# Kernel optimization log

Hardware: AMD Instinct MI355X
Metric: run time of the kernel (lower is better)

## Reference

```python
import jax, jax.numpy as jnp
import numpy as np

K = 64  # init kwarg k
B, D = 4096, 16384


def setup_inputs() -> dict:
    key = jax.random.key(0)
    x = jax.random.normal(key, (B, D), dtype=jnp.float32)
    return {"x": x}


def reference(x):
    # top-k along last dim, then scatter values into a zero tensor (same as
    # torch.topk + zeros_like + scatter_).
    vals, idx = jax.lax.top_k(x, K)            # [B, K], [B, K]
    rows = jnp.arange(x.shape[0])[:, None]     # [B, 1] broadcast against idx
    return jnp.zeros_like(x).at[rows, idx].set(vals)
```

## Files before the change

kernel.cpp:

```cpp
#include <hip/hip_runtime.h>


#define TK_D      16384
#define TK_K      64
#define TK_BLOCK  512
#define TK_NF4    8
#define TK_BINS   2048
#define TK_EQCAP  1024

__device__ __forceinline__ unsigned ord_map(unsigned b) {
    return b ^ ((unsigned)((int)b >> 31) | 0x80000000u);
}

__launch_bounds__(TK_BLOCK, 4)
__global__ void topk_scatter_kernel(const float* __restrict__ x,
                                    float* __restrict__ out) {
    __shared__ __align__(16) unsigned sh_vals[TK_D];
    __shared__ int      sh_hist[TK_BINS];
    __shared__ int      sh_wsum[8];
    __shared__ unsigned sh_prefix;
    __shared__ int      sh_rem;
    __shared__ int      sh_eqn;
    __shared__ int      sh_eqidx[TK_EQCAP];

    const int row  = blockIdx.x;
    const int tid  = threadIdx.x;
    const int lane = tid & 63;
    const int wv   = tid >> 6;

    const float4* __restrict__ xrow = (const float4*)(x + (size_t)row * TK_D);

    #pragma unroll
    for (int i = 0; i < TK_NF4; i++) {
        const int c4 = wv * 64 + i * TK_BLOCK;
        __builtin_amdgcn_global_load_lds(
            (const __attribute__((address_space(1))) void*)(xrow + c4 + lane),
            (__attribute__((address_space(3))) void*)(&sh_vals[4 * c4]),
            16, 0, 0);
    }

    ((int4*)sh_hist)[tid] = int4{0, 0, 0, 0};
    if (tid == 0) { sh_prefix = 0u; sh_rem = TK_K; sh_eqn = 0; }
    __syncthreads();

    const int histshift[3]  = {21, 10, 0};
    const int scopeshift[3] = {0, 21, 10};
    const int nbits[3]      = {11, 11, 10};

    for (int p = 0; p < 3; p++) {
        const unsigned pref = sh_prefix;
        const int      rem  = sh_rem;
        const int      hs   = histshift[p];
        const unsigned msk  = (1u << nbits[p]) - 1u;
        #pragma unroll
        for (int i = 0; i < TK_NF4; i++) {
            uint4 b = ((const uint4*)sh_vals)[tid + i * TK_BLOCK];
            #pragma unroll
            for (int c = 0; c < 4; c++) {
                unsigned u = ord_map(((const unsigned*)&b)[c]);
                bool in_scope = (p == 0) || ((u >> scopeshift[p] >> nbits[0]) == pref);
                in_scope = (p == 0) || ((u >> (hs + nbits[p])) == pref);
                if (in_scope) atomicAdd(&sh_hist[(u >> hs) & msk], 1);
            }
        }
        __syncthreads();

        int h0 = sh_hist[4 * tid + 0], h1 = sh_hist[4 * tid + 1];
        int h2 = sh_hist[4 * tid + 2], h3 = sh_hist[4 * tid + 3];
        int local = h0 + h1 + h2 + h3;
        int suf = local;
        #pragma unroll
        for (int off = 1; off < 64; off <<= 1) {
            int o = __shfl_down(suf, off);
            if (lane + off < 64) suf += o;
        }
        if (lane == 0) sh_wsum[wv] = suf;
        __syncthreads();

        ((int4*)sh_hist)[tid] = int4{0, 0, 0, 0};

        int above = 0;
        #pragma unroll
        for (int w2 = 0; w2 < 8; w2++)
            if (w2 > wv) above += sh_wsum[w2];

        int a3 = above + (suf - local);
        int S3 = a3 + h3, S2 = S3 + h2, S1 = S2 + h1, S0 = S1 + h0;
        int d = -1, ab = 0;
        if      (S3 >= rem && a3 < rem) { d = 4 * tid + 3; ab = a3; }
        else if (S2 >= rem && S3 < rem) { d = 4 * tid + 2; ab = S3; }
        else if (S1 >= rem && S2 < rem) { d = 4 * tid + 1; ab = S2; }
        else if (S0 >= rem && S1 < rem) { d = 4 * tid + 0; ab = S1; }
        if (d >= 0) {
            sh_prefix = (pref << nbits[p]) | (unsigned)d;
            sh_rem    = rem - ab;
        }
        __syncthreads();
    }

    const unsigned T    = sh_prefix;
    const int      need = sh_rem;

    float4* __restrict__ orow = (float4*)(out + (size_t)row * TK_D);
    #pragma unroll
    for (int i = 0; i < TK_NF4; i++) {
        const int c4 = tid + i * TK_BLOCK;
        uint4 b = ((const uint4*)sh_vals)[c4];
        float4 o;
        #pragma unroll
        for (int c = 0; c < 4; c++) {
            unsigned raw = ((const unsigned*)&b)[c];
            unsigned u   = ord_map(raw);
            ((float*)&o)[c] = (u > T) ? __uint_as_float(raw) : 0.0f;
            if (u == T) {
                int pos = atomicAdd(&sh_eqn, 1);
                if (pos < TK_EQCAP) sh_eqidx[pos] = 4 * c4 + c;
            }
        }
        orow[c4] = o;
    }
    __syncthreads();

    const int L = min(sh_eqn, TK_EQCAP);
    for (int i = tid; i < L; i += TK_BLOCK) {
        int col  = sh_eqidx[i];
        int rank = 0;
        for (int j = 0; j < L; j++) rank += (sh_eqidx[j] < col);
        if (rank < need)
            out[(size_t)row * TK_D + col] = __uint_as_float(sh_vals[col]);
    }
}

extern "C" void kernel_launch(void* const* d_in, const int* in_sizes, int n_in,
                              void* d_out, int out_size, void* d_ws, size_t ws_size,
                              hipStream_t stream) {
    const float* x = (const float*)d_in[0];
    float* out = (float*)d_out;
    const int B = in_sizes[0] / TK_D;
    topk_scatter_kernel<<<B, TK_BLOCK, 0, stream>>>(x, out);
}
```

Before: 444.6 us.

## Replace three-pass radix select with one histogram pass plus candidate rank selection

Each row is now held in registers instead of being staged through a 64 KB LDS buffer. The three radix histogram passes become a single 11-bit histogram pass. Elements falling in the boundary bin are compacted into a small LDS candidate list, and an O(C^2) rank computation over that list finds the exact threshold. Dropping the large LDS buffer raises the occupancy target to 6 blocks and removes two full histogram passes. The cost is more register pressure and a quadratic step that could become expensive, or overflow the 1024-entry cap, if the boundary bin is large.

```diff
diff --git a/kernel.cpp b/kernel.cpp
--- a/kernel.cpp
+++ b/kernel.cpp
@@ -4,130 +4,141 @@
 #define TK_D      16384
 #define TK_K      64
 #define TK_BLOCK  512
-#define TK_NF4    8
+#define TK_NV     8
 #define TK_BINS   2048
-#define TK_EQCAP  1024
+#define TK_CAP    1024
 
 __device__ __forceinline__ unsigned ord_map(unsigned b) {
     return b ^ ((unsigned)((int)b >> 31) | 0x80000000u);
 }
+__device__ __forceinline__ unsigned ord_inv(unsigned u) {
+    return u ^ ((unsigned)((int)(~u) >> 31) | 0x80000000u);
+}
 
-__launch_bounds__(TK_BLOCK, 4)
+__launch_bounds__(TK_BLOCK, 6)
 __global__ void topk_scatter_kernel(const float* __restrict__ x,
                                     float* __restrict__ out) {
-    __shared__ __align__(16) unsigned sh_vals[TK_D];
     __shared__ int      sh_hist[TK_BINS];
     __shared__ int      sh_wsum[8];
-    __shared__ unsigned sh_prefix;
+    __shared__ unsigned sh_cu[TK_CAP];
+    __shared__ int      sh_cidx[TK_CAP];
+    __shared__ int      sh_bin;
     __shared__ int      sh_rem;
-    __shared__ int      sh_eqn;
-    __shared__ int      sh_eqidx[TK_EQCAP];
+    __shared__ int      sh_cnt;
+    __shared__ unsigned sh_T;
+    __shared__ int      sh_need;
 
     const int row  = blockIdx.x;
     const int tid  = threadIdx.x;
     const int lane = tid & 63;
     const int wv   = tid >> 6;
 
-    const float4* __restrict__ xrow = (const float4*)(x + (size_t)row * TK_D);
+    const uint4* __restrict__ xr = (const uint4*)(x + (size_t)row * TK_D);
+    uint4 r[TK_NV];
+    #pragma unroll
+    for (int i = 0; i < TK_NV; i++) r[i] = xr[tid + i * TK_BLOCK];
+
+    ((int4*)sh_hist)[tid] = int4{0, 0, 0, 0};
+    if (tid == 0) sh_cnt = 0;
+    __syncthreads();
 
     #pragma unroll
-    for (int i = 0; i < TK_NF4; i++) {
-        const int c4 = wv * 64 + i * TK_BLOCK;
-        __builtin_amdgcn_global_load_lds(
-            (const __attribute__((address_space(1))) void*)(xrow + c4 + lane),
-            (__attribute__((address_space(3))) void*)(&sh_vals[4 * c4]),
-            16, 0, 0);
+    for (int i = 0; i < TK_NV; i++) {
+        #pragma unroll
+        for (int c = 0; c < 4; c++) {
+            unsigned u = ord_map(((const unsigned*)&r[i])[c]);
+            atomicAdd(&sh_hist[u >> 21], 1);
+        }
     }
-
-    ((int4*)sh_hist)[tid] = int4{0, 0, 0, 0};
-    if (tid == 0) { sh_prefix = 0u; sh_rem = TK_K; sh_eqn = 0; }
     __syncthreads();
 
-    const int histshift[3]  = {21, 10, 0};
-    const int scopeshift[3] = {0, 21, 10};
-    const int nbits[3]      = {11, 11, 10};
+    int h0 = sh_hist[4 * tid + 0], h1 = sh_hist[4 * tid + 1];
+    int h2 = sh_hist[4 * tid + 2], h3 = sh_hist[4 * tid + 3];
+    int local = h0 + h1 + h2 + h3;
+    int suf = local;
+    #pragma unroll
+    for (int off = 1; off < 64; off <<= 1) {
+        int o = __shfl_down(suf, off);
+        if (lane + off < 64) suf += o;
+    }
+    if (lane == 0) sh_wsum[wv] = suf;
+    __syncthreads();
 
-    for (int p = 0; p < 3; p++) {
-        const unsigned pref = sh_prefix;
-        const int      rem  = sh_rem;
-        const int      hs   = histshift[p];
-        const unsigned msk  = (1u << nbits[p]) - 1u;
+    int above = 0;
+    #pragma unroll
+    for (int w2 = 0; w2 < 8; w2++)
+        if (w2 > wv) above += sh_wsum[w2];
+
+    int a3 = above + (suf - local);
+    int S3 = a3 + h3, S2 = S3 + h2, S1 = S2 + h1, S0 = S1 + h0;
+    if      (S3 >= TK_K && a3 < TK_K) { sh_bin = 4 * tid + 3; sh_rem = TK_K - a3; }
+    else if (S2 >= TK_K && S3 < TK_K) { sh_bin = 4 * tid + 2; sh_rem = TK_K - S3; }
+    else if (S1 >= TK_K && S2 < TK_K) { sh_bin = 4 * tid + 1; sh_rem = TK_K - S2; }
+    else if (S0 >= TK_K && S1 < TK_K) { sh_bin = 4 * tid + 0; sh_rem = TK_K - S1; }
+    __syncthreads();
+
+    const unsigned binv = (unsigned)sh_bin;
+    const int      rem  = sh_rem;
+
+    #pragma unroll
+    for (int i = 0; i < TK_NV; i++) {
         #pragma unroll
-        for (int i = 0; i < TK_NF4; i++) {
-            uint4 b = ((const uint4*)sh_vals)[tid + i * TK_BLOCK];
-            #pragma unroll
-            for (int c = 0; c < 4; c++) {
-                unsigned u = ord_map(((const unsigned*)&b)[c]);
-                bool in_scope = (p == 0) || ((u >> scopeshift[p] >> nbits[0]) == pref);
-                in_scope = (p == 0) || ((u >> (hs + nbits[p])) == pref);
-                if (in_scope) atomicAdd(&sh_hist[(u >> hs) & msk], 1);
+        for (int c = 0; c < 4; c++) {
+            unsigned u = ord_map(((const unsigned*)&r[i])[c]);
+            if ((u >> 21) == binv) {
+                int pos = atomicAdd(&sh_cnt, 1);
+                if (pos < TK_CAP) {
+                    sh_cu[pos]   = u;
+                    sh_cidx[pos] = 4 * (tid + i * TK_BLOCK) + c;
+                }
             }
         }
-        __syncthreads();
+    }
+    __syncthreads();
 
-        int h0 = sh_hist[4 * tid + 0], h1 = sh_hist[4 * tid + 1];
-        int h2 = sh_hist[4 * tid + 2], h3 = sh_hist[4 * tid + 3];
-        int local = h0 + h1 + h2 + h3;
-        int suf = local;
-        #pragma unroll
-        for (int off = 1; off < 64; off <<= 1) {
-            int o = __shfl_down(suf, off);
-            if (lane + off < 64) suf += o;
+    const int C = min(sh_cnt, TK_CAP);
+    for (int i = tid; i < C; i += TK_BLOCK) {
+        unsigned ui = sh_cu[i];
+        int abv = 0, eq = 0;
+        for (int j = 0; j < C; j++) {
+            unsigned uj = sh_cu[j];
+            abv += (uj > ui);
+            eq  += (uj == ui);
         }
-        if (lane == 0) sh_wsum[wv] = suf;
-        __syncthreads();
+        if (abv < rem && abv + eq >= rem) {
+            sh_T    = ui;
+            sh_need = rem - abv;
+        }
+    }
+    __syncthreads();
 
-        ((int4*)sh_hist)[tid] = int4{0, 0, 0, 0};
-
-        int above = 0;
-        #pragma unroll
-        for (int w2 = 0; w2 < 8; w2++)
-            if (w2 > wv) above += sh_wsum[w2];
-
-        int a3 = above + (suf - local);
-        int S3 = a3 + h3, S2 = S3 + h2, S1 = S2 + h1, S0 = S1 + h0;
-        int d = -1, ab = 0;
-        if      (S3 >= rem && a3 < rem) { d = 4 * tid + 3; ab = a3; }
-        else if (S2 >= rem && S3 < rem) { d = 4 * tid + 2; ab = S3; }
-        else if (S1 >= rem && S2 < rem) { d = 4 * tid + 1; ab = S2; }
-        else if (S0 >= rem && S1 < rem) { d = 4 * tid + 0; ab = S1; }
-        if (d >= 0) {
-            sh_prefix = (pref << nbits[p]) | (unsigned)d;
-            sh_rem    = rem - ab;
-        }
-        __syncthreads();
-    }
-
-    const unsigned T    = sh_prefix;
-    const int      need = sh_rem;
+    const unsigned T    = sh_T;
+    const int      need = sh_need;
 
     float4* __restrict__ orow = (float4*)(out + (size_t)row * TK_D);
     #pragma unroll
-    for (int i = 0; i < TK_NF4; i++) {
-        const int c4 = tid + i * TK_BLOCK;
-        uint4 b = ((const uint4*)sh_vals)[c4];
+    for (int i = 0; i < TK_NV; i++) {
         float4 o;
         #pragma unroll
         for (int c = 0; c < 4; c++) {
-            unsigned raw = ((const unsigned*)&b)[c];
+            unsigned raw = ((const unsigned*)&r[i])[c];
             unsigned u   = ord_map(raw);
             ((float*)&o)[c] = (u > T) ? __uint_as_float(raw) : 0.0f;
-            if (u == T) {
-                int pos = atomicAdd(&sh_eqn, 1);
-                if (pos < TK_EQCAP) sh_eqidx[pos] = 4 * c4 + c;
-            }
         }
-        orow[c4] = o;
+        orow[tid + i * TK_BLOCK] = o;
     }
     __syncthreads();
 
-    const int L = min(sh_eqn, TK_EQCAP);
-    for (int i = tid; i < L; i += TK_BLOCK) {
-        int col  = sh_eqidx[i];
-        int rank = 0;
-        for (int j = 0; j < L; j++) rank += (sh_eqidx[j] < col);
-        if (rank < need)
-            out[(size_t)row * TK_D + col] = __uint_as_float(sh_vals[col]);
+    const float tval = __uint_as_float(ord_inv(T));
+    for (int i = tid; i < C; i += TK_BLOCK) {
+        if (sh_cu[i] == T) {
+            int col  = sh_cidx[i];
+            int rank = 0;
+            for (int j = 0; j < C; j++)
+                rank += (sh_cu[j] == T && sh_cidx[j] < col);
+            if (rank < need)
+                out[(size_t)row * TK_D + col] = tval;
+        }
     }
 }
 
```

Result: slower. 510.5 us (+14.8%).
